# Kernel tuning notes

Measured on AMD Instinct MI355X. Metric: run time of the kernel, lower is better.

Reference implementation:

```python
import jax, jax.numpy as jnp
import numpy as np

B, S, W = 64, 128, 16
E, H = 256, 512
WV, CV, NC = 50000, 128, 20


def _lstm(x, lens, Wih, Whh, b):
    """Masked LSTM over padded sequences.
    x: [N,T,D], lens: [N] int. Returns (ys [N,T,Hd] zeroed past lens, h_last [N,Hd]).
    Gate layout [i,f,g,o] as in PyTorch; b = b_ih + b_hh fused.
    """
    N, T, _ = x.shape
    Hd = Whh.shape[1]

    def step(carry, inp):
        h, c = carry
        xt, t = inp
        z = xt @ Wih.T + h @ Whh.T + b  # [N,4Hd]
        i, f, g, o = jnp.split(z, 4, axis=-1)
        c_new = jax.nn.sigmoid(f) * c + jax.nn.sigmoid(i) * jnp.tanh(g)
        h_new = jax.nn.sigmoid(o) * jnp.tanh(c_new)
        m = (t < lens)[:, None]
        h = jnp.where(m, h_new, h)  # freeze state past sequence end (packed semantics)
        c = jnp.where(m, c_new, c)
        return (h, c), jnp.where(m, h, 0.0)

    h0 = jnp.zeros((N, Hd), x.dtype)
    (h, _), ys = jax.lax.scan(step, (h0, h0), (jnp.swapaxes(x, 0, 1), jnp.arange(T)))
    return jnp.swapaxes(ys, 0, 1), h


def _rev_pad(x, lens):
    """Reverse each sequence within its valid length; padding stays in place."""
    T = x.shape[1]
    t = jnp.arange(T)[None, :]
    idx = jnp.where(t < lens[:, None], lens[:, None] - 1 - t, t)
    return jnp.take_along_axis(x, idx[:, :, None], axis=1)


def setup_inputs() -> dict:
    key = jax.random.key(0)
    ks = jax.random.split(key, 16)
    sc = 0.05
    words = jax.random.randint(ks[0], (B, S), 0, WV)
    words_num = jax.random.randint(ks[1], (B,), 1, S + 1)
    chars = jax.random.randint(ks[2], (B, S, W), 0, CV)
    char_lens = jax.random.randint(ks[3], (B, S), 1, W + 1)
    word_emb = jax.random.normal(ks[4], (WV, E)) * sc
    char_emb = jax.random.normal(ks[5], (CV, E)) * sc
    l0_Wih = jax.random.normal(ks[6], (2, 4 * H, E)) * sc
    l0_Whh = jax.random.normal(ks[7], (2, 4 * H, H)) * sc
    l0_b = jax.random.normal(ks[8], (2, 4 * H)) * sc
    l1_Wih = jax.random.normal(ks[9], (2, 4 * H, 2 * H)) * sc
    l1_Whh = jax.random.normal(ks[10], (2, 4 * H, H)) * sc
    l1_b = jax.random.normal(ks[11], (2, 4 * H)) * sc
    c_Wih = jax.random.normal(ks[12], (4 * (2 * H), E)) * sc
    c_Whh = jax.random.normal(ks[13], (4 * (2 * H), 2 * H)) * sc
    c_b = jax.random.normal(ks[14], (4 * (2 * H),)) * sc
    lin_W = jax.random.normal(ks[15], (NC, 2 * H)) * sc
    lin_b = jnp.zeros((NC,))
    return dict(words=words, words_num=words_num, chars=chars, char_lens=char_lens,
                word_emb=word_emb, char_emb=char_emb,
                l0_Wih=l0_Wih, l0_Whh=l0_Whh, l0_b=l0_b,
                l1_Wih=l1_Wih, l1_Whh=l1_Whh, l1_b=l1_b,
                c_Wih=c_Wih, c_Whh=c_Whh, c_b=c_b,
                lin_W=lin_W, lin_b=lin_b)


def reference(words, words_num, chars, char_lens, word_emb, char_emb,
              l0_Wih, l0_Whh, l0_b, l1_Wih, l1_Whh, l1_b,
              c_Wih, c_Whh, c_b, lin_W, lin_b):
    # word path: embedding + 2-layer bidirectional LSTM (packed -> masked)
    h = word_emb[words]  # [B,S,E]
    for Wih, Whh, b in ((l0_Wih, l0_Whh, l0_b), (l1_Wih, l1_Whh, l1_b)):
        fwd, _ = _lstm(h, words_num, Wih[0], Whh[0], b[0])
        bwd, _ = _lstm(_rev_pad(h, words_num), words_num, Wih[1], Whh[1], b[1])
        h = jnp.concatenate([fwd, _rev_pad(bwd, words_num)], axis=-1)  # [B,S,2H]

    # char path: one batched LSTM over all B*S words (collapses per-sentence loop)
    b_, s_, w_ = chars.shape
    ce = char_emb[chars.reshape(b_ * s_, w_)]  # [B*S,W,E]
    _, hc = _lstm(ce, char_lens.reshape(b_ * s_), c_Wih, c_Whh, c_b)  # final h_n [B*S,2H]
    y = hc.reshape(b_, s_, -1)
    valid = (jnp.arange(s_)[None, :] < words_num[:, None])[..., None]
    y = jnp.where(valid, y, 0.0)  # pad_sequence pads missing words with zeros

    return (h + y) @ lin_W.T + lin_b  # [B,S,NC]
```

## Files before the change

kernel.cpp:

```cpp
#include <hip/hip_runtime.h>
#include <stdint.h>

#define SLEN 128
#define NW 8192
#define WCH 16
#define EDIM 256
#define HDIM 512
#define G4 2048
#define CH 1024
#define CG 4096
#define NCLS 20

typedef __attribute__((ext_vector_type(4))) float f32x4;
typedef __attribute__((ext_vector_type(8))) short s16x8;

__device__ __forceinline__ ushort f2b(float f){
  uint32_t u = __float_as_uint(f);
  return (ushort)((u + 0x7FFFu + ((u>>16)&1u)) >> 16);
}
__device__ __forceinline__ float b2f(ushort s){ return __uint_as_float(((uint32_t)s)<<16); }
__device__ __forceinline__ float sigf(float x){ return 1.f/(1.f+__expf(-x)); }
__device__ __forceinline__ float tanhf_(float x){
  float t = fminf(fmaxf(2.f*x,-30.f),30.f);
  float e = __expf(t);
  return (e-1.f)/(e+1.f);
}

__device__ __forceinline__ void gl16(const ushort* g, ushort* l){
  __builtin_amdgcn_global_load_lds((const __attribute__((address_space(1))) uint32_t*)g,
                                   (__attribute__((address_space(3))) uint32_t*)l, 16, 0, 0);
}

__global__ void k_fill(uint32_t* __restrict__ p, uint32_t v, int n){
  int i = blockIdx.x*256 + threadIdx.x;
  if (i < n) p[i] = v;
}

__global__ void k_cvt(const float* __restrict__ s, ushort* __restrict__ d, int n){
  int i = blockIdx.x*256 + threadIdx.x;
  if (i < n) d[i] = f2b(s[i]);
}

__global__ void k_cwhhp(const float* __restrict__ s, ushort* __restrict__ d){
  int i = blockIdx.x*256 + threadIdx.x;
  int dr = i >> 10, k = i & 1023;
  int nb = dr >> 7, w7 = dr & 127;
  int g = w7 >> 5, wn = (w7>>4)&1, hl = w7&15;
  int h = nb*32 + wn*16 + hl;
  d[i] = f2b(s[(size_t)(g*1024 + h)*1024 + k]);
}

__global__ void k_wwhhp(const float* __restrict__ s, ushort* __restrict__ d){
  int i = blockIdx.x*256 + threadIdx.x;
  int dr = i >> 9, k = i & 511;
  int dir = dr >> 11; int r = dr & 2047;
  int y = r >> 7, w7 = r & 127;
  int g = w7 >> 5, wn = (w7>>4)&1, hl = w7&15;
  int h = y*32 + wn*16 + hl;
  d[i] = f2b(s[((size_t)dir*2048 + g*512 + h)*512 + k]);
}

__global__ void k_emb(const int* __restrict__ words, const float* __restrict__ we,
                      ushort* __restrict__ d){
  int i = blockIdx.x*256 + threadIdx.x;
  int w = i >> 8, e = i & 255;
  d[i] = f2b(we[(size_t)words[w]*EDIM + e]);
}

__global__ void k_cproj(const float* __restrict__ cemb, const float* __restrict__ cwih,
                        const float* __restrict__ cb, float* __restrict__ out){
  int i = blockIdx.x*256 + threadIdx.x;
  int c = i >> 12, p = i & 4095;
  int nb = p >> 7, w7 = p & 127;
  int g = w7>>5, wn = (w7>>4)&1, hl = w7&15;
  int j = g*1024 + nb*32 + wn*16 + hl;
  const float* a = cemb + (size_t)c*EDIM;
  const float* b = cwih + (size_t)j*EDIM;
  float acc = cb[j];
  for (int k=0;k<EDIM;k+=4){
    float4 av = *(const float4*)&a[k]; float4 bv = *(const float4*)&b[k];
    acc += av.x*bv.x + av.y*bv.y + av.z*bv.z + av.w*bv.w;
  }
  out[i] = acc;
}

__global__ void k_hist(const int* __restrict__ wn, const int* __restrict__ cl,
                       int* __restrict__ cnt17){
  int w = blockIdx.x*256 + threadIdx.x; if (w >= NW) return;
  int b = w >> 7, s = w & 127;
  if (s < wn[b]) atomicAdd(&cnt17[cl[w]], 1);
}

__global__ void k_scan(const int* __restrict__ cnt17, int* __restrict__ cnt_step,
                       int* __restrict__ cur){
  if (threadIdx.x==0 && blockIdx.x==0){
    cnt_step[16] = 0;
    for (int t=15;t>=0;t--) cnt_step[t] = cnt_step[t+1] + cnt17[t+1];
    for (int l=1;l<=16;l++) cur[l] = cnt_step[l];
  }
}

__global__ void k_scatter(const int* __restrict__ wn, const int* __restrict__ cl,
                          const int* __restrict__ chars, int* __restrict__ cur,
                          int* __restrict__ inv, int* __restrict__ chperm){
  int w = blockIdx.x*256 + threadIdx.x; if (w >= NW) return;
  int b = w >> 7, s = w & 127;
  if (s < wn[b]){
    int len = cl[w];
    int pos = atomicAdd(&cur[len], 1);
    inv[w] = pos;
    for (int j=0;j<WCH;j++) chperm[pos*WCH + j] = chars[w*WCH + j];
  }
}

template<int EPI>
__global__ __launch_bounds__(256) void k_gemm(
    const ushort* __restrict__ A, int ldA,
    const ushort* __restrict__ Bm, int ldB, size_t bStrideZ,
    ushort* __restrict__ outX, const float* __restrict__ bias,
    size_t oStrideZ, size_t biasStrideZ, int K,
    const int* __restrict__ cnt_step, int tstep,
    const int* __restrict__ chperm, const float* __restrict__ cproj,
    float* __restrict__ ccell, ushort* __restrict__ hcdst)
{
  int cntv = 0;
  if (EPI==1){ cntv = cnt_step[tstep]; if ((int)(blockIdx.x*128) >= cntv) return; }
  __shared__ __align__(16) ushort As[128*64];
  __shared__ __align__(16) ushort Bs[128*64];
  int tid = threadIdx.x, wid = tid>>6, lane = tid&63;
  int wm = wid>>1, wn = wid&1;
  int l15 = lane&15, l4 = lane>>4;
  const ushort* Ab = A + (size_t)blockIdx.x*128*ldA;
  const ushort* Bb = Bm + (size_t)blockIdx.z*bStrideZ + (size_t)blockIdx.y*128*ldB;
  f32x4 acc[4][4];
  #pragma unroll
  for (int i=0;i<4;i++)
    #pragma unroll
    for (int j=0;j<4;j++) acc[i][j] = f32x4{0.f,0.f,0.f,0.f};

  for (int k0=0; k0<K; k0+=64){
    #pragma unroll
    for (int i=0;i<4;i++){
      int fcb = (i*4 + wid)*64;
      int fc = fcb + lane;
      int row = fc>>3, cp = fc&7, c = cp ^ (row&7);
      gl16(Ab + (size_t)row*ldA + k0 + c*8, As + fcb*8);
    }
    #pragma unroll
    for (int i=0;i<4;i++){
      int fcb = (i*4 + wid)*64;
      int fc = fcb + lane;
      int row = fc>>3, cp = fc&7, c = cp ^ (row&7);
      gl16(Bb + (size_t)row*ldB + k0 + c*8, Bs + fcb*8);
    }
    __syncthreads();
    #pragma unroll
    for (int kw=0; kw<2; kw++){
      s16x8 af[4], bfr[4];
      #pragma unroll
      for (int mf=0; mf<4; mf++){
        int r = wm*64 + mf*16 + l15;
        int slot = (kw*4 + l4) ^ (r&7);
        af[mf] = *(const s16x8*)&As[r*64 + slot*8];
      }
      #pragma unroll
      for (int nf=0; nf<4; nf++){
        int r = (EPI==1) ? (nf*32 + wn*16 + l15) : (wn*64 + nf*16 + l15);
        int slot = (kw*4 + l4) ^ (r&7);
        bfr[nf] = *(const s16x8*)&Bs[r*64 + slot*8];
      }
      #pragma unroll
      for (int mf=0; mf<4; mf++)
        #pragma unroll
        for (int nf=0; nf<4; nf++)
          acc[mf][nf] = __builtin_amdgcn_mfma_f32_16x16x32_bf16(af[mf], bfr[nf], acc[mf][nf], 0,0,0);
    }
    __syncthreads();
  }

  if (EPI==0){
    ushort* op = outX + blockIdx.z*oStrideZ;
    const float* bp = bias + blockIdx.z*biasStrideZ;
    #pragma unroll
    for (int mf=0; mf<4; mf++){
      #pragma unroll
      for (int r=0;r<4;r++){
        int row = blockIdx.x*128 + wm*64 + mf*16 + l4*4 + r;
        #pragma unroll
        for (int nf=0;nf<4;nf++){
          int col = blockIdx.y*128 + wn*64 + nf*16 + l15;
          op[(size_t)row*G4 + col] = f2b(acc[mf][nf][r] + bp[col]);
        }
      }
    }
  } else {
    int hb = blockIdx.y*32 + wn*16 + l15;
    #pragma unroll
    for (int mf=0; mf<4; mf++){
      #pragma unroll
      for (int r=0;r<4;r++){
        int row = blockIdx.x*128 + wm*64 + mf*16 + l4*4 + r;
        if (row < cntv){
          int cid = chperm[row*WCH + tstep];
          const float* cp = cproj + (size_t)cid*CG + blockIdx.y*128 + wn*16 + l15;
          float zi = acc[mf][0][r] + cp[0];
          float zf = acc[mf][1][r] + cp[32];
          float zg = acc[mf][2][r] + cp[64];
          float zo = acc[mf][3][r] + cp[96];
          size_t ix = (size_t)row*CH + hb;
          float c = ccell[ix];
          float cn = sigf(zf)*c + sigf(zi)*tanhf_(zg);
          ccell[ix] = cn;
          hcdst[ix] = f2b(sigf(zo)*tanhf_(cn));
        }
      }
    }
  }
}

__global__ __launch_bounds__(256) void k_wrec(
    ushort* __restrict__ hbuf,
    const ushort* __restrict__ X,
    const ushort* __restrict__ Wp,
    const int* __restrict__ lens,
    ushort* __restrict__ outcat,
    int* __restrict__ bar)
{
  __shared__ __align__(16) ushort Ws[8*128*64];
  __shared__ __align__(16) ushort As[64*64];
  int tid = threadIdx.x, wid = tid>>6, lane = tid&63;
  int l15 = lane&15, l4 = lane>>4;
  int y = blockIdx.x & 15, dir = blockIdx.x >> 4;
  const ushort* Wb = Wp + ((size_t)dir*2048 + (size_t)y*128)*512;

  #pragma unroll
  for (int kt=0; kt<8; ++kt)
    #pragma unroll
    for (int i=0;i<4;i++){
      int fcb = (i*4 + wid)*64;
      int fc = fcb + lane;
      int row = fc>>3, cp = fc&7, c = cp ^ (row&7);
      gl16(Wb + (size_t)row*512 + kt*64 + c*8, Ws + kt*8192 + fcb*8);
    }
  asm volatile("s_waitcnt vmcnt(0)" ::: "memory");
  __builtin_amdgcn_sched_barrier(0);
  __builtin_amdgcn_s_barrier();

  int b0 = wid*16 + l4*4;
  int lenv[4];
  #pragma unroll
  for (int r=0;r<4;r++) lenv[r] = lens[b0+r];
  float  cacc[2][4];
  ushort hprev[2][4];
  #pragma unroll
  for (int wn=0;wn<2;wn++)
    #pragma unroll
    for (int r=0;r<4;r++){ cacc[wn][r]=0.f; hprev[wn][r]=0; }

  int* mybar = bar + dir;

  for (int t=0;t<SLEN;t++){
    const ushort* hsrc = hbuf + ((size_t)((t&1)*2 + dir))*32768;
    ushort*       hdst = hbuf + ((size_t)((((t&1)^1))*2 + dir))*32768;
    f32x4 acc[8];
    #pragma unroll
    for (int n=0;n<8;n++) acc[n] = f32x4{0.f,0.f,0.f,0.f};

    for (int kt=0; kt<8; ++kt){
      #pragma unroll
      for (int i=0;i<2;i++){
        int fcb = (i*4 + wid)*64;
        int fc = fcb + lane;
        int row = fc>>3, cp = fc&7, c = cp ^ (row&7);
        gl16(hsrc + (size_t)row*512 + kt*64 + c*8, As + fcb*8);
      }
      asm volatile("s_waitcnt vmcnt(0)" ::: "memory");
      __builtin_amdgcn_sched_barrier(0);
      __builtin_amdgcn_s_barrier();
      #pragma unroll
      for (int kw=0; kw<2; kw++){
        s16x8 af;
        { int r = wid*16 + l15; int slot = (kw*4 + l4) ^ (r&7);
          af = *(const s16x8*)&As[r*64 + slot*8]; }
        #pragma unroll
        for (int nf=0; nf<8; nf++){
          int r = nf*16 + l15; int slot = (kw*4 + l4) ^ (r&7);
          s16x8 bfr = *(const s16x8*)&Ws[kt*8192 + r*64 + slot*8];
          acc[nf] = __builtin_amdgcn_mfma_f32_16x16x32_bf16(af, bfr, acc[nf], 0,0,0);
        }
      }
      __builtin_amdgcn_s_barrier();
    }

    #pragma unroll
    for (int wn=0;wn<2;wn++){
      int h = y*32 + wn*16 + l15;
      #pragma unroll
      for (int r=0;r<4;r++){
        int b = b0 + r;
        ushort hnew;
        if (t < lenv[r]){
          int pos = dir ? (lenv[r]-1-t) : t;
          size_t xbase = ((size_t)dir*NW + (size_t)b*SLEN + pos)*G4 + h;
          float zi = acc[0+wn][r] + b2f(X[xbase]);
          float zf = acc[2+wn][r] + b2f(X[xbase + 512]);
          float zg = acc[4+wn][r] + b2f(X[xbase + 1024]);
          float zo = acc[6+wn][r] + b2f(X[xbase + 1536]);
          float cn = sigf(zf)*cacc[wn][r] + sigf(zi)*tanhf_(zg);
          cacc[wn][r] = cn;
          float hv = sigf(zo)*tanhf_(cn);
          hnew = f2b(hv);
          outcat[((size_t)b*SLEN + pos)*1024 + dir*HDIM + h] = hnew;
        } else {
          hnew = hprev[wn][r];
        }
        hprev[wn][r] = hnew;
        hdst[(size_t)b*512 + h] = hnew;
      }
    }

    __syncthreads();
    if (tid==0){
      __threadfence();
      __hip_atomic_fetch_add(mybar, 1, __ATOMIC_RELEASE, __HIP_MEMORY_SCOPE_AGENT);
      int tgt = 16*(t+1);
      while (__hip_atomic_load(mybar, __ATOMIC_ACQUIRE, __HIP_MEMORY_SCOPE_AGENT) < tgt)
        __builtin_amdgcn_s_sleep(8);
      __threadfence();
    }
    __syncthreads();
  }
}

__global__ void k_gather(const ushort* __restrict__ hc0, const ushort* __restrict__ hc1,
                         const int* __restrict__ inv, const int* __restrict__ cl,
                         ushort* __restrict__ ycat){
  int i = blockIdx.x*256 + threadIdx.x;
  if (i >= NW*128) return;
  int w = i >> 7, seg = i & 127;
  int iv = inv[w];
  ulonglong2 z; z.x = 0; z.y = 0;
  if (iv >= 0){
    const ushort* src = (((cl[w]-1)&1) ? hc0 : hc1) + (size_t)iv*CH + seg*8;
    z = *(const ulonglong2*)src;
  }
  *(ulonglong2*)(ycat + (size_t)w*CH + seg*8) = z;
}

__global__ __launch_bounds__(256) void k_final(
    const ushort* __restrict__ h1cat, const ushort* __restrict__ ycat,
    const float* __restrict__ lw, const float* __restrict__ lb,
    float* __restrict__ out)
{
  int i = blockIdx.x*256 + threadIdx.x;
  if (i >= NW*NCLS) return;
  int w = i / NCLS, o = i - w*NCLS;
  const ushort* hr = h1cat + (size_t)w*1024;
  const ushort* yr = ycat  + (size_t)w*1024;
  const float* wr = lw + (size_t)o*1024;
  float acc = lb[o];
  for (int k=0;k<1024;k+=4){
    float4 wv = *(const float4*)&wr[k];
    ushort4 a4 = *(const ushort4*)&hr[k];
    ushort4 b4 = *(const ushort4*)&yr[k];
    acc += (b2f(a4.x)+b2f(b4.x))*wv.x + (b2f(a4.y)+b2f(b4.y))*wv.y
         + (b2f(a4.z)+b2f(b4.z))*wv.z + (b2f(a4.w)+b2f(b4.w))*wv.w;
  }
  out[i] = acc;
}

extern "C" void kernel_launch(void* const* d_in, const int* in_sizes, int n_in,
                              void* d_out, int out_size, void* d_ws, size_t ws_size,
                              hipStream_t stream)
{
  const int*   words = (const int*)d_in[0];
  const int*   wnum  = (const int*)d_in[1];
  const int*   chars = (const int*)d_in[2];
  const int*   clens = (const int*)d_in[3];
  const float* wemb  = (const float*)d_in[4];
  const float* cemb  = (const float*)d_in[5];
  const float* l0Wih = (const float*)d_in[6];
  const float* l0Whh = (const float*)d_in[7];
  const float* l0b   = (const float*)d_in[8];
  const float* l1Wih = (const float*)d_in[9];
  const float* l1Whh = (const float*)d_in[10];
  const float* l1b   = (const float*)d_in[11];
  const float* cWih  = (const float*)d_in[12];
  const float* cWhh  = (const float*)d_in[13];
  const float* cb    = (const float*)d_in[14];
  const float* linW  = (const float*)d_in[15];
  const float* linb  = (const float*)d_in[16];
  float* out = (float*)d_out;

  char* base = (char*)d_ws;
  const size_t MB = (size_t)1<<20;
  ushort* hc0    = (ushort*)(base);
  ushort* hc1    = (ushort*)(base + 16*MB);
  float*  ccell  = (float*) (base + 32*MB);
  ushort* X      = (ushort*)(base);
  ushort* cwp    = (ushort*)(base + 64*MB);
  ushort* l1w    = (ushort*)(base + 64*MB);
  float*  cproj  = (float*) (base + 72*MB);
  int*    chperm = (int*)   (base + 74*MB);
  ushort* embw   = (ushort*)(base + 72*MB);
  ushort* w1p    = (ushort*)(base + 72*MB);
  ushort* ycat   = (ushort*)(base + 76*MB);
  ushort* h0cat  = (ushort*)(base + 92*MB);
  ushort* h1cat  = (ushort*)(base + 92*MB);
  ushort* l0w    = (ushort*)(base + 108*MB);
  ushort* w0p    = (ushort*)(base + 110*MB);
  ushort* hbuf   = (ushort*)(base + 114*MB);
  int*    bar    = (int*)   (base + 114*MB + 256*1024);
  int*    inv    = (int*)   (base + 114*MB + 512*1024);
  int*    cnt17  = (int*)   (base + 114*MB + 544*1024);
  int*    cntstep= (int*)   (base + 114*MB + 545*1024);
  int*    cur    = (int*)   (base + 114*MB + 546*1024);

  k_fill<<<1, 256, 0, stream>>>((uint32_t*)cnt17, 0u, 17);
  k_fill<<<(NW+255)/256, 256, 0, stream>>>((uint32_t*)inv, 0xFFFFFFFFu, NW);
  k_fill<<<(NW*CH/2+255)/256, 256, 0, stream>>>((uint32_t*)hc0, 0u, NW*CH/2);
  k_fill<<<(NW*CH+255)/256, 256, 0, stream>>>((uint32_t*)ccell, 0u, NW*CH);
  k_cwhhp<<<(CG*CH)/256, 256, 0, stream>>>(cWhh, cwp);
  k_cproj<<<(128*CG)/256, 256, 0, stream>>>(cemb, cWih, cb, cproj);
  k_hist<<<NW/256, 256, 0, stream>>>(wnum, clens, cnt17);
  k_scan<<<1, 1, 0, stream>>>(cnt17, cntstep, cur);
  k_scatter<<<NW/256, 256, 0, stream>>>(wnum, clens, chars, cur, inv, chperm);

  for (int t=0;t<WCH;t++){
    const ushort* hs = (t&1)? hc1 : hc0;
    ushort*       hd = (t&1)? hc0 : hc1;
    k_gemm<1><<<dim3(64,32,1), 256, 0, stream>>>(hs, CH, cwp, CH, 0,
        nullptr, nullptr, 0, 0, CH,
        cntstep, t, chperm, cproj, ccell, hd);
  }
  k_gather<<<(NW*128+255)/256, 256, 0, stream>>>(hc0, hc1, inv, clens, ycat);

  k_cvt<<<(2*G4*EDIM+255)/256, 256, 0, stream>>>(l0Wih, l0w, 2*G4*EDIM);
  k_cvt<<<(2*G4*1024+255)/256, 256, 0, stream>>>(l1Wih, l1w, 2*G4*1024);
  k_wwhhp<<<(2*G4*HDIM)/256, 256, 0, stream>>>(l0Whh, w0p);
  k_emb<<<(NW*EDIM)/256, 256, 0, stream>>>(words, wemb, embw);
  k_fill<<<(NW*512+255)/256, 256, 0, stream>>>((uint32_t*)h0cat, 0u, NW*512);
  k_fill<<<(32768+255)/256, 256, 0, stream>>>((uint32_t*)hbuf, 0u, 32768);
  k_fill<<<1, 256, 0, stream>>>((uint32_t*)bar, 0u, 2);

  k_gemm<0><<<dim3(64,16,2), 256, 0, stream>>>(embw, EDIM, l0w, EDIM, (size_t)G4*EDIM,
      X, l0b, (size_t)NW*G4, (size_t)G4, EDIM,
      nullptr, 0, nullptr, nullptr, nullptr, nullptr);

  k_wwhhp<<<(2*G4*HDIM)/256, 256, 0, stream>>>(l1Whh, w1p);

  k_wrec<<<32, 256, 0, stream>>>(hbuf, X, w0p, wnum, h0cat, bar);

  k_gemm<0><<<dim3(64,16,2), 256, 0, stream>>>(h0cat, 1024, l1w, 1024, (size_t)G4*1024,
      X, l1b, (size_t)NW*G4, (size_t)G4, 1024,
      nullptr, 0, nullptr, nullptr, nullptr, nullptr);

  k_fill<<<(NW*512+255)/256, 256, 0, stream>>>((uint32_t*)h1cat, 0u, NW*512);
  k_fill<<<(32768+255)/256, 256, 0, stream>>>((uint32_t*)hbuf, 0u, 32768);
  k_fill<<<1, 256, 0, stream>>>((uint32_t*)bar, 0u, 2);

  k_wrec<<<32, 256, 0, stream>>>(hbuf, X, w1p, wnum, h1cat, bar);

  k_final<<<(NW*NCLS+255)/256, 256, 0, stream>>>(h1cat, ycat, linW, linb, out);
}
```

Baseline: 4.432 ms.

## Load recurrent h directly into registers and relax grid barrier ordering

The word-LSTM recurrent kernel no longer stages h through shared memory in eight k-tiles with block barriers. Each lane now loads its whole A-fragment row for all of K with agent-scope relaxed atomic loads up front, and h is written back with relaxed atomic stores. The cross-block barrier drops its thread fences and acquire/release ordering in favour of a vmcnt wait and relaxed atomics, and it polls with a shorter sleep. This removes per-tile LDS round trips and intra-block syncs and lowers per-step barrier latency, but it relies on relaxed atomics giving cache-coherent visibility, which adds a memory-ordering correctness risk.

```diff
diff --git a/kernel.cpp b/kernel.cpp
--- a/kernel.cpp
+++ b/kernel.cpp
@@ -227,7 +227,6 @@
     int* __restrict__ bar)
 {
   __shared__ __align__(16) ushort Ws[8*128*64];
-  __shared__ __align__(16) ushort As[64*64];
   int tid = threadIdx.x, wid = tid>>6, lane = tid&63;
   int l15 = lane&15, l4 = lane>>4;
   int y = blockIdx.x & 15, dir = blockIdx.x >> 4;
@@ -246,6 +245,7 @@
   __builtin_amdgcn_sched_barrier(0);
   __builtin_amdgcn_s_barrier();
 
+  int arow = wid*16 + l15;
   int b0 = wid*16 + l4*4;
   int lenv[4];
   #pragma unroll
@@ -258,39 +258,36 @@
     for (int r=0;r<4;r++){ cacc[wn][r]=0.f; hprev[wn][r]=0; }
 
   int* mybar = bar + dir;
+  union Q2V { unsigned long long q[2]; s16x8 v; };
 
   for (int t=0;t<SLEN;t++){
-    const ushort* hsrc = hbuf + ((size_t)((t&1)*2 + dir))*32768;
-    ushort*       hdst = hbuf + ((size_t)((((t&1)^1))*2 + dir))*32768;
+    const ushort* hs = hbuf + ((size_t)((t&1)*2 + dir))*32768;
+    ushort*       hd = hbuf + ((size_t)(((t&1)^1)*2 + dir))*32768;
+
+    const ushort* hrow = hs + (size_t)arow*512 + l4*8;
+    unsigned long long q0[16], q1[16];
+    #pragma unroll
+    for (int f=0; f<16; ++f){
+      const unsigned long long* p = (const unsigned long long*)(hrow + f*32);
+      q0[f] = __hip_atomic_load(p,   __ATOMIC_RELAXED, __HIP_MEMORY_SCOPE_AGENT);
+      q1[f] = __hip_atomic_load(p+1, __ATOMIC_RELAXED, __HIP_MEMORY_SCOPE_AGENT);
+    }
+
     f32x4 acc[8];
     #pragma unroll
     for (int n=0;n<8;n++) acc[n] = f32x4{0.f,0.f,0.f,0.f};
-
-    for (int kt=0; kt<8; ++kt){
-      #pragma unroll
-      for (int i=0;i<2;i++){
-        int fcb = (i*4 + wid)*64;
-        int fc = fcb + lane;
-        int row = fc>>3, cp = fc&7, c = cp ^ (row&7);
-        gl16(hsrc + (size_t)row*512 + kt*64 + c*8, As + fcb*8);
-      }
-      asm volatile("s_waitcnt vmcnt(0)" ::: "memory");
-      __builtin_amdgcn_sched_barrier(0);
-      __builtin_amdgcn_s_barrier();
-      #pragma unroll
-      for (int kw=0; kw<2; kw++){
-        s16x8 af;
-        { int r = wid*16 + l15; int slot = (kw*4 + l4) ^ (r&7);
-          af = *(const s16x8*)&As[r*64 + slot*8]; }
+    #pragma unroll
+    for (int kt=0; kt<8; ++kt)
+      #pragma unroll
+      for (int kw=0; kw<2; ++kw){
+        Q2V u; u.q[0]=q0[kt*2+kw]; u.q[1]=q1[kt*2+kw];
         #pragma unroll
         for (int nf=0; nf<8; nf++){
-          int r = nf*16 + l15; int slot = (kw*4 + l4) ^ (r&7);
-          s16x8 bfr = *(const s16x8*)&Ws[kt*8192 + r*64 + slot*8];
-          acc[nf] = __builtin_amdgcn_mfma_f32_16x16x32_bf16(af, bfr, acc[nf], 0,0,0);
+          int rr = nf*16 + l15; int slot = (kw*4 + l4) ^ (rr&7);
+          s16x8 bfr = *(const s16x8*)&Ws[kt*8192 + rr*64 + slot*8];
+          acc[nf] = __builtin_amdgcn_mfma_f32_16x16x32_bf16(u.v, bfr, acc[nf], 0,0,0);
         }
       }
-      __builtin_amdgcn_s_barrier();
-    }
 
     #pragma unroll
     for (int wn=0;wn<2;wn++){
@@ -315,18 +312,18 @@
           hnew = hprev[wn][r];
         }
         hprev[wn][r] = hnew;
-        hdst[(size_t)b*512 + h] = hnew;
-      }
-    }
-
+        __hip_atomic_store(&hd[(size_t)b*512 + h], hnew,
+                           __ATOMIC_RELAXED, __HIP_MEMORY_SCOPE_AGENT);
+      }
+    }
+
+    asm volatile("s_waitcnt vmcnt(0)" ::: "memory");
     __syncthreads();
     if (tid==0){
-      __threadfence();
-      __hip_atomic_fetch_add(mybar, 1, __ATOMIC_RELEASE, __HIP_MEMORY_SCOPE_AGENT);
+      __hip_atomic_fetch_add(mybar, 1, __ATOMIC_RELAXED, __HIP_MEMORY_SCOPE_AGENT);
       int tgt = 16*(t+1);
-      while (__hip_atomic_load(mybar, __ATOMIC_ACQUIRE, __HIP_MEMORY_SCOPE_AGENT) < tgt)
-        __builtin_amdgcn_s_sleep(8);
-      __threadfence();
+      while (__hip_atomic_load(mybar, __ATOMIC_RELAXED, __HIP_MEMORY_SCOPE_AGENT) < tgt)
+        __builtin_amdgcn_s_sleep(2);
     }
     __syncthreads();
   }
```

Result: slower. 4.676 ms (+5.5%).
